# Optimization experiments

Measured on AMD Instinct MI355X. Metric: run time of the kernel, lower is better.

Reference implementation:

```python
import jax, jax.numpy as jnp
import numpy as np

B, N, T, DM, H, M = 32, 207, 24, 64, 8, 32
E = 2 * DM  # true input feature dim (2*dmodel per the reshape in the source)


def setup_inputs() -> dict:
    rng = jax.random.key(0)
    ks = jax.random.split(rng, 10)
    s = 0.05  # scale params to keep activations numerically sane
    query = jax.random.normal(ks[0], (B, N, T, E), jnp.float32)
    key = jax.random.normal(ks[1], (B, N, T, E), jnp.float32)
    value = jax.random.normal(ks[2], (B, N, T, E), jnp.float32)
    # causal temporal mask, broadcast over batch/node/head; True = masked out
    atten_mask = jnp.broadcast_to(jnp.triu(jnp.ones((T, T), bool), 1), (B, N, 1, T, T))
    qp1 = jax.random.normal(ks[3], (N * DM, M), jnp.float32) * s
    qp2 = jax.random.normal(ks[4], (M, 4 * DM), jnp.float32) * s
    kp1 = jax.random.normal(ks[5], (N * DM, M), jnp.float32) * s
    kp2 = jax.random.normal(ks[6], (M, 4 * DM), jnp.float32) * s
    vp1 = jax.random.normal(ks[7], (N * DM, M), jnp.float32) * s
    vp2 = jax.random.normal(ks[8], (M, 4 * DM), jnp.float32) * s
    out_W = jax.random.normal(ks[9], (E, DM), jnp.float32) * s
    out_b = jnp.zeros((DM,), jnp.float32)
    return dict(query=query, key=key, value=value, atten_mask=atten_mask,
                qp1=qp1, qp2=qp2, kp1=kp1, kp2=kp2, vp1=vp1, vp2=vp2,
                out_W=out_W, out_b=out_b, num_heads=H)


def reference(query, key, value, atten_mask, qp1, qp2, kp1, kp2, vp1, vp2, out_W, out_b, num_heads):
    b, n, t, e = query.shape

    def proj(x, p1, p2):
        # low-rank factored per-node projection: (N*dmodel, M) @ (M, 4*dmodel) -> (N, E, E)
        P = (p1 @ p2).reshape(n, e, e)
        y = jnp.einsum('bnti,nik->bntk', x, P)
        return jax.nn.relu(y).reshape(b, n, t, num_heads, -1)

    q = proj(query, qp1, qp2)   # (B,N,T,H,d)
    k = proj(key, kp1, kp2)
    v = proj(value, vp1, vp2)

    scale = 1.0 / np.sqrt(q.shape[-1]).astype(np.float32)
    scores = jnp.einsum('bnthe,bnshe->bnhts', q, k)          # (B,N,H,T,S)
    scores = jnp.where(atten_mask, -jnp.inf, scores)          # masked_fill before scaling
    attn = jax.nn.softmax(scale * scores, axis=-1)            # dropout disabled (eval)
    out = jnp.einsum('bnhts,bnshd->bnthd', attn, v).reshape(b, n, t, -1)
    out = jax.nn.relu(out @ out_W + out_b)                    # (B,N,T,dmodel)
    return out, attn
```

## Files before the change

### kernel.cpp

```cpp
#include <hip/hip_runtime.h>
#include <hip/hip_bf16.h>

#define Bn 32
#define Nn 207
#define Tt 24
#define Ee 128
#define Hh 8
#define Dm 64
#define Mm 32
#define NBN (Bn * Nn)
#define PT ((size_t)Nn * 16384)

typedef __attribute__((ext_vector_type(8))) short bf16x8;
typedef __attribute__((ext_vector_type(4))) float f32x4;

__device__ __forceinline__ unsigned swz256(unsigned a) { return a ^ (((a >> 8) & 7u) << 4); }
__device__ __forceinline__ unsigned swz64(unsigned a)  { return a ^ (((a >> 7) & 3u) << 4); }
__device__ __forceinline__ unsigned f2b(float f) {
  union { float f; unsigned u; } x; x.f = f;
  unsigned u = x.u;
  return ((u + 0x7FFFu + ((u >> 16) & 1u)) >> 16) & 0xFFFFu;
}

__global__ __launch_bounds__(256) void build_P_frag3(
    const float* __restrict__ qp1, const float* __restrict__ qp2,
    const float* __restrict__ kp1, const float* __restrict__ kp2,
    const float* __restrict__ vp1, const float* __restrict__ vp2,
    unsigned short* __restrict__ Pt) {
  const int tau = blockIdx.y;
  const float* p1 = (tau == 0) ? qp1 : (tau == 1) ? kp1 : vp1;
  const float* p2 = (tau == 0) ? qp2 : (tau == 1) ? kp2 : vp2;
  unsigned short* dst = Pt + (size_t)tau * PT;
  const int bid = blockIdx.x;
  const int n = bid >> 3;
  const int r8 = bid & 7;
  const int ks = r8 >> 1;
  const int chunk = ((r8 & 1) << 1) + (threadIdx.x >> 7);
  const int col = threadIdx.x & 127;
  const int base_i = ks * 32 + chunk * 8;
  const float* p1r = p1 + (size_t)(n * 64 + (base_i >> 1)) * Mm;
  const float* p2a = p2 + col;
  const float* p2b = p2 + 128 + col;
  float acc[8] = {};
#pragma unroll
  for (int m = 0; m < Mm; ++m) {
    float a = p2a[m * 256], b = p2b[m * 256];
#pragma unroll
    for (int jj = 0; jj < 4; ++jj) {
      float pv = p1r[jj * Mm + m];
      acc[2 * jj]     = fmaf(pv, a, acc[2 * jj]);
      acc[2 * jj + 1] = fmaf(pv, b, acc[2 * jj + 1]);
    }
  }
  const int nt = col >> 4;
  const int lane = (chunk << 4) | (col & 15);
  union { unsigned short u[8]; uint4 v; } w;
#pragma unroll
  for (int j = 0; j < 8; ++j) w.u[j] = (unsigned short)f2b(acc[j]);
  *(uint4*)(dst + (size_t)(((n * 8 + nt) * 4 + ks) * 64 + lane) * 8) = w.v;
}

__global__ __launch_bounds__(256) void build_W_frag(const float* __restrict__ W,
                                                    unsigned short* __restrict__ Wt) {
  for (int idx = threadIdx.x; idx < 1024; idx += 256) {
    int lane = idx & 63, ks = (idx >> 6) & 3, nt = idx >> 8;
    union { unsigned short u[8]; uint4 v; } w;
#pragma unroll
    for (int j = 0; j < 8; ++j)
      w.u[j] = (unsigned short)f2b(W[(size_t)(ks * 32 + (lane >> 4) * 8 + j) * 64 + nt * 16 + (lane & 15)]);
    *(uint4*)(Wt + (size_t)idx * 8) = w.v;
  }
}

__global__ __launch_bounds__(256, 4) void fused_attn(
    const float* __restrict__ Qin, const float* __restrict__ Kin,
    const float* __restrict__ Vin,
    const unsigned short* __restrict__ Ptq, const unsigned short* __restrict__ Ptk,
    const unsigned short* __restrict__ Ptv, const unsigned short* __restrict__ Wt,
    const float* __restrict__ bias,
    float* __restrict__ out, float* __restrict__ attn) {
  __shared__ __align__(16) char smem[32768];
  const int tid = threadIdx.x;
  const int lane = tid & 63;
  const int wv = tid >> 6;
  const int c = lane & 15;
  const int g = lane >> 4;
  const f32x4 zf = {0.f, 0.f, 0.f, 0.f};
  const bf16x8 zb = {0, 0, 0, 0, 0, 0, 0, 0};

  int bx = blockIdx.x;
  bx = (bx & 7) * 828 + (bx >> 3);
  const int n = bx >> 5;
  const int b = bx & 31;
  const size_t xbase = (size_t)(b * Nn + n) * (Tt * Ee);

  {
    uint4 z4 = {0, 0, 0, 0};
    *(uint4*)(smem + 24576 + tid * 32) = z4;
    *(uint4*)(smem + 24576 + tid * 32 + 16) = z4;
    const float* src[2] = {Qin + xbase, Kin + xbase};
#pragma unroll
    for (int w = 0; w < 2; ++w)
#pragma unroll
      for (int it = 0; it < 3; ++it) {
        int e4 = tid + 256 * it;
        float4 xv = *(const float4*)(src[w] + (size_t)e4 * 4);
        unsigned a = swz256((unsigned)((e4 >> 5) * 256 + (e4 & 31) * 8));
        uint2 pk;
        pk.x = f2b(xv.x) | (f2b(xv.y) << 16);
        pk.y = f2b(xv.z) | (f2b(xv.w) << 16);
        *(uint2*)(smem + w * 6144 + a) = pk;
      }
  }
  __syncthreads();

  {
    const unsigned short* Pts[2] = {Ptq, Ptk};
#pragma unroll
    for (int w = 0; w < 2; ++w) {
      const unsigned short* Pf = Pts[w];
      f32x4 acc[2][2] = {{zf, zf}, {zf, zf}};
#pragma unroll
      for (int ks = 0; ks < 4; ++ks) {
        bf16x8 Bf[2], Af[2];
#pragma unroll
        for (int ntl = 0; ntl < 2; ++ntl)
          Bf[ntl] = *(const bf16x8*)(Pf + (size_t)(((n * 8 + (wv * 2 + ntl)) * 4 + ks) * 64 + lane) * 8);
#pragma unroll
        for (int mt = 0; mt < 2; ++mt) {
          int row = mt * 16 + c; row = row < 24 ? row : 23;
          Af[mt] = *(const bf16x8*)(smem + w * 6144 + swz256((unsigned)(row * 256 + ks * 64 + g * 16)));
        }
        __builtin_amdgcn_s_setprio(1);
#pragma unroll
        for (int mt = 0; mt < 2; ++mt)
#pragma unroll
          for (int ntl = 0; ntl < 2; ++ntl)
            acc[mt][ntl] = __builtin_amdgcn_mfma_f32_16x16x32_bf16(Af[mt], Bf[ntl], acc[mt][ntl], 0, 0, 0);
        __builtin_amdgcn_s_setprio(0);
      }
      const float postscale = (w == 0) ? 0.25f : 1.0f;
      char* dst = smem + 12288 + w * 6144;
#pragma unroll
      for (int mt = 0; mt < 2; ++mt)
#pragma unroll
        for (int r = 0; r < 4; ++r) {
          int row = mt * 16 + g * 4 + r;
          if (row < 24) {
#pragma unroll
            for (int ntl = 0; ntl < 2; ++ntl) {
              int col = (wv * 2 + ntl) * 16 + c;
              *(unsigned short*)(dst + swz256((unsigned)(row * 256 + col * 2))) =
                  (unsigned short)f2b(fmaxf(acc[mt][ntl][r], 0.f) * postscale);
            }
          }
        }
    }
  }

  float4 xvr[3];
#pragma unroll
  for (int it = 0; it < 3; ++it)
    xvr[it] = *(const float4*)(Vin + xbase + (size_t)(tid + 256 * it) * 4);
  __syncthreads();

  f32x4 sc[2][2][2];
#pragma unroll
  for (int hh = 0; hh < 2; ++hh) {
    int h = wv * 2 + hh;
    bf16x8 Aq[2], Bk[2];
#pragma unroll
    for (int mt = 0; mt < 2; ++mt) {
      int row = mt * 16 + c; row = row < 24 ? row : 23;
      Aq[mt] = zb;
      if (lane < 32) Aq[mt] = *(const bf16x8*)(smem + 12288 + swz256((unsigned)(row * 256 + (h * 16 + g * 8) * 2)));
    }
#pragma unroll
    for (int st = 0; st < 2; ++st) {
      int row = st * 16 + c; row = row < 24 ? row : 23;
      Bk[st] = zb;
      if (lane < 32) Bk[st] = *(const bf16x8*)(smem + 18432 + swz256((unsigned)(row * 256 + (h * 16 + g * 8) * 2)));
    }
    __builtin_amdgcn_s_setprio(1);
#pragma unroll
    for (int mt = 0; mt < 2; ++mt)
#pragma unroll
      for (int st = 0; st < 2; ++st)
        sc[hh][mt][st] = __builtin_amdgcn_mfma_f32_16x16x32_bf16(Aq[mt], Bk[st], zf, 0, 0, 0);
    __builtin_amdgcn_s_setprio(0);
  }
  __syncthreads();

  {
    const size_t abase = (size_t)(b * Nn + n) * (Hh * Tt * Tt);
#pragma unroll
    for (int hh = 0; hh < 2; ++hh) {
      int h = wv * 2 + hh;
#pragma unroll
      for (int mt = 0; mt < 2; ++mt)
#pragma unroll
        for (int r = 0; r < 4; ++r) {
          int t = mt * 16 + g * 4 + r;
          float e0 = (c <= t)      ? __expf(sc[hh][mt][0][r]) : 0.f;
          float e1 = (16 + c <= t) ? __expf(sc[hh][mt][1][r]) : 0.f;
          float s2 = e0 + e1;
          s2 += __shfl_xor(s2, 1);
          s2 += __shfl_xor(s2, 2);
          s2 += __shfl_xor(s2, 4);
          s2 += __shfl_xor(s2, 8);
          float inv = 1.0f / s2;
          float p0 = e0 * inv, p1 = e1 * inv;
          if (t < 24) {
            float* ap = attn + abase + (size_t)h * (Tt * Tt) + t * Tt;
            ap[c] = p0;
            if (c < 8) ap[16 + c] = p1;
            char* q = smem + 12288;
            *(unsigned short*)(q + swz64((unsigned)(h * 1536 + t * 64 + c * 2)))        = (unsigned short)f2b(p0);
            *(unsigned short*)(q + swz64((unsigned)(h * 1536 + t * 64 + (16 + c) * 2))) = (unsigned short)f2b(p1);
          }
        }
    }
#pragma unroll
    for (int it = 0; it < 3; ++it) {
      int e4 = tid + 256 * it;
      unsigned a = swz256((unsigned)((e4 >> 5) * 256 + (e4 & 31) * 8));
      uint2 pk;
      pk.x = f2b(xvr[it].x) | (f2b(xvr[it].y) << 16);
      pk.y = f2b(xvr[it].z) | (f2b(xvr[it].w) << 16);
      *(uint2*)(smem + 6144 + a) = pk;
    }
  }
  __syncthreads();

  {
    f32x4 acc[2][2] = {{zf, zf}, {zf, zf}};
#pragma unroll
    for (int ks = 0; ks < 4; ++ks) {
      bf16x8 Bf[2], Af[2];
#pragma unroll
      for (int ntl = 0; ntl < 2; ++ntl)
        Bf[ntl] = *(const bf16x8*)(Ptv + (size_t)(((n * 8 + (wv * 2 + ntl)) * 4 + ks) * 64 + lane) * 8);
#pragma unroll
      for (int mt = 0; mt < 2; ++mt) {
        int row = mt * 16 + c; row = row < 24 ? row : 23;
        Af[mt] = *(const bf16x8*)(smem + 6144 + swz256((unsigned)(row * 256 + ks * 64 + g * 16)));
      }
      __builtin_amdgcn_s_setprio(1);
#pragma unroll
      for (int mt = 0; mt < 2; ++mt)
#pragma unroll
        for (int ntl = 0; ntl < 2; ++ntl)
          acc[mt][ntl] = __builtin_amdgcn_mfma_f32_16x16x32_bf16(Af[mt], Bf[ntl], acc[mt][ntl], 0, 0, 0);
      __builtin_amdgcn_s_setprio(0);
    }
#pragma unroll
    for (int mt = 0; mt < 2; ++mt)
#pragma unroll
      for (int r = 0; r < 4; ++r) {
        int srow = mt * 16 + g * 4 + r;
        if (srow < 24) {
#pragma unroll
          for (int ntl = 0; ntl < 2; ++ntl) {
            int dcol = (wv * 2 + ntl) * 16 + c;
            *(unsigned short*)(smem + 24576 + swz64((unsigned)(dcol * 64 + srow * 2))) =
                (unsigned short)f2b(fmaxf(acc[mt][ntl][r], 0.f));
          }
        }
      }
  }
  __syncthreads();

  {
    f32x4 pv[2][2];
#pragma unroll
    for (int hh = 0; hh < 2; ++hh) {
      int h = wv * 2 + hh;
      bf16x8 Bv = *(const bf16x8*)(smem + 24576 + swz64((unsigned)((h * 16 + c) * 64 + g * 16)));
#pragma unroll
      for (int mt = 0; mt < 2; ++mt) {
        int row = mt * 16 + c; row = row < 24 ? row : 23;
        bf16x8 Ap = *(const bf16x8*)(smem + 12288 + swz64((unsigned)(h * 1536 + row * 64 + g * 16)));
        pv[hh][mt] = __builtin_amdgcn_mfma_f32_16x16x32_bf16(Ap, Bv, zf, 0, 0, 0);
      }
    }
#pragma unroll
    for (int hh = 0; hh < 2; ++hh) {
      int h = wv * 2 + hh;
#pragma unroll
      for (int mt = 0; mt < 2; ++mt)
#pragma unroll
        for (int r = 0; r < 4; ++r) {
          int t = mt * 16 + g * 4 + r;
          if (t < 24)
            *(unsigned short*)(smem + swz256((unsigned)(t * 256 + (h * 16 + c) * 2))) =
                (unsigned short)f2b(pv[hh][mt][r]);
        }
    }
  }
  __syncthreads();

  {
    f32x4 acc2[2] = {zf, zf};
#pragma unroll
    for (int ks = 0; ks < 4; ++ks) {
      bf16x8 Bw = *(const bf16x8*)(Wt + (size_t)((wv * 4 + ks) * 64 + lane) * 8);
      bf16x8 Af[2];
#pragma unroll
      for (int mt = 0; mt < 2; ++mt) {
        int row = mt * 16 + c; row = row < 24 ? row : 23;
        Af[mt] = *(const bf16x8*)(smem + swz256((unsigned)(row * 256 + ks * 64 + g * 16)));
      }
      __builtin_amdgcn_s_setprio(1);
#pragma unroll
      for (int mt = 0; mt < 2; ++mt)
        acc2[mt] = __builtin_amdgcn_mfma_f32_16x16x32_bf16(Af[mt], Bw, acc2[mt], 0, 0, 0);
      __builtin_amdgcn_s_setprio(0);
    }
    int j = wv * 16 + c;
    float bj = bias[j];
    const size_t obase = (size_t)(b * Nn + n) * (Tt * Dm);
#pragma unroll
    for (int mt = 0; mt < 2; ++mt)
#pragma unroll
      for (int r = 0; r < 4; ++r) {
        int t = mt * 16 + g * 4 + r;
        if (t < 24) out[obase + (size_t)t * Dm + j] = fmaxf(acc2[mt][r] + bj, 0.f);
      }
  }
}

extern "C" void kernel_launch(void* const* d_in, const int* in_sizes, int n_in,
                              void* d_out, int out_size, void* d_ws, size_t ws_size,
                              hipStream_t stream) {
  const float* query = (const float*)d_in[0];
  const float* key   = (const float*)d_in[1];
  const float* value = (const float*)d_in[2];
  const float* qp1 = (const float*)d_in[4];
  const float* qp2 = (const float*)d_in[5];
  const float* kp1 = (const float*)d_in[6];
  const float* kp2 = (const float*)d_in[7];
  const float* vp1 = (const float*)d_in[8];
  const float* vp2 = (const float*)d_in[9];
  const float* out_W = (const float*)d_in[10];
  const float* out_b = (const float*)d_in[11];

  unsigned short* Pt  = (unsigned short*)d_ws;
  unsigned short* Wtf = Pt + 3 * PT;

  float* out = (float*)d_out;
  float* attn = out + (size_t)NBN * Tt * Dm;

  build_P_frag3<<<dim3(Nn * 8, 3), 256, 0, stream>>>(qp1, qp2, kp1, kp2, vp1, vp2, Pt);
  build_W_frag<<<1, 256, 0, stream>>>(out_W, Wtf);
  fused_attn<<<NBN, 256, 0, stream>>>(query, key, value,
                                      Pt, Pt + PT, Pt + 2 * PT, Wtf,
                                      out_b, out, attn);
}
```

Measured before the change: 159.2 us.

## Fuse V projection into QK projection stage and use hardware bf16 pack converts

```diff
diff --git a/kernel.cpp b/kernel.cpp
--- a/kernel.cpp
+++ b/kernel.cpp
@@ -16,10 +16,13 @@
 
 __device__ __forceinline__ unsigned swz256(unsigned a) { return a ^ (((a >> 8) & 7u) << 4); }
 __device__ __forceinline__ unsigned swz64(unsigned a)  { return a ^ (((a >> 7) & 3u) << 4); }
-__device__ __forceinline__ unsigned f2b(float f) {
-  union { float f; unsigned u; } x; x.f = f;
-  unsigned u = x.u;
-  return ((u + 0x7FFFu + ((u >> 16) & 1u)) >> 16) & 0xFFFFu;
+__device__ __forceinline__ unsigned cvtpk(float lo, float hi) {
+  unsigned r;
+  asm("v_cvt_pk_bf16_f32 %0, %1, %2" : "=v"(r) : "v"(lo), "v"(hi));
+  return r;
+}
+__device__ __forceinline__ unsigned short f2bs(float f) {
+  return (unsigned short)cvtpk(f, f);
 }
 
 __global__ __launch_bounds__(256) void build_P_frag3(
@@ -54,9 +57,9 @@
   }
   const int nt = col >> 4;
   const int lane = (chunk << 4) | (col & 15);
-  union { unsigned short u[8]; uint4 v; } w;
-#pragma unroll
-  for (int j = 0; j < 8; ++j) w.u[j] = (unsigned short)f2b(acc[j]);
+  union { unsigned u[4]; uint4 v; } w;
+#pragma unroll
+  for (int jj = 0; jj < 4; ++jj) w.u[jj] = cvtpk(acc[2 * jj], acc[2 * jj + 1]);
   *(uint4*)(dst + (size_t)(((n * 8 + nt) * 4 + ks) * 64 + lane) * 8) = w.v;
 }
 
@@ -64,10 +67,13 @@
                                                     unsigned short* __restrict__ Wt) {
   for (int idx = threadIdx.x; idx < 1024; idx += 256) {
     int lane = idx & 63, ks = (idx >> 6) & 3, nt = idx >> 8;
-    union { unsigned short u[8]; uint4 v; } w;
-#pragma unroll
-    for (int j = 0; j < 8; ++j)
-      w.u[j] = (unsigned short)f2b(W[(size_t)(ks * 32 + (lane >> 4) * 8 + j) * 64 + nt * 16 + (lane & 15)]);
+    union { unsigned u[4]; uint4 v; } w;
+#pragma unroll
+    for (int jj = 0; jj < 4; ++jj) {
+      float a = W[(size_t)(ks * 32 + (lane >> 4) * 8 + 2 * jj) * 64 + nt * 16 + (lane & 15)];
+      float b = W[(size_t)(ks * 32 + (lane >> 4) * 8 + 2 * jj + 1) * 64 + nt * 16 + (lane & 15)];
+      w.u[jj] = cvtpk(a, b);
+    }
     *(uint4*)(Wt + (size_t)idx * 8) = w.v;
   }
 }
@@ -79,7 +85,7 @@
     const unsigned short* __restrict__ Ptv, const unsigned short* __restrict__ Wt,
     const float* __restrict__ bias,
     float* __restrict__ out, float* __restrict__ attn) {
-  __shared__ __align__(16) char smem[32768];
+  __shared__ __align__(16) char smem[38912];
   const int tid = threadIdx.x;
   const int lane = tid & 63;
   const int wv = tid >> 6;
@@ -96,29 +102,28 @@
 
   {
     uint4 z4 = {0, 0, 0, 0};
-    *(uint4*)(smem + 24576 + tid * 32) = z4;
-    *(uint4*)(smem + 24576 + tid * 32 + 16) = z4;
-    const float* src[2] = {Qin + xbase, Kin + xbase};
-#pragma unroll
-    for (int w = 0; w < 2; ++w)
+    *(uint4*)(smem + 30720 + tid * 32) = z4;
+    *(uint4*)(smem + 30720 + tid * 32 + 16) = z4;
+    const float* src[3] = {Qin + xbase, Kin + xbase, Vin + xbase};
+#pragma unroll
+    for (int w = 0; w < 3; ++w)
 #pragma unroll
       for (int it = 0; it < 3; ++it) {
         int e4 = tid + 256 * it;
         float4 xv = *(const float4*)(src[w] + (size_t)e4 * 4);
         unsigned a = swz256((unsigned)((e4 >> 5) * 256 + (e4 & 31) * 8));
         uint2 pk;
-        pk.x = f2b(xv.x) | (f2b(xv.y) << 16);
-        pk.y = f2b(xv.z) | (f2b(xv.w) << 16);
+        pk.x = cvtpk(xv.x, xv.y);
+        pk.y = cvtpk(xv.z, xv.w);
         *(uint2*)(smem + w * 6144 + a) = pk;
       }
   }
   __syncthreads();
 
   {
-    const unsigned short* Pts[2] = {Ptq, Ptk};
-#pragma unroll
-    for (int w = 0; w < 2; ++w) {
-      const unsigned short* Pf = Pts[w];
+#pragma unroll
+    for (int w = 0; w < 3; ++w) {
+      const unsigned short* Pf = (w == 0) ? Ptq : (w == 1) ? Ptk : Ptv;
       f32x4 acc[2][2] = {{zf, zf}, {zf, zf}};
 #pragma unroll
       for (int ks = 0; ks < 4; ++ks) {
@@ -139,55 +144,40 @@
             acc[mt][ntl] = __builtin_amdgcn_mfma_f32_16x16x32_bf16(Af[mt], Bf[ntl], acc[mt][ntl], 0, 0, 0);
         __builtin_amdgcn_s_setprio(0);
       }
-      const float postscale = (w == 0) ? 0.25f : 1.0f;
-      char* dst = smem + 12288 + w * 6144;
-#pragma unroll
-      for (int mt = 0; mt < 2; ++mt)
-#pragma unroll
-        for (int r = 0; r < 4; ++r) {
-          int row = mt * 16 + g * 4 + r;
-          if (row < 24) {
-#pragma unroll
-            for (int ntl = 0; ntl < 2; ++ntl) {
-              int col = (wv * 2 + ntl) * 16 + c;
-              *(unsigned short*)(dst + swz256((unsigned)(row * 256 + col * 2))) =
-                  (unsigned short)f2b(fmaxf(acc[mt][ntl][r], 0.f) * postscale);
+      if (w < 2) {
+        const float postscale = (w == 0) ? 0.25f : 1.0f;
+        char* dst = smem + 18432 + w * 6144;
+#pragma unroll
+        for (int mt = 0; mt < 2; ++mt)
+#pragma unroll
+          for (int r = 0; r < 4; ++r) {
+            int row = mt * 16 + g * 4 + r;
+            if (row < 24) {
+#pragma unroll
+              for (int ntl = 0; ntl < 2; ++ntl) {
+                int col = (wv * 2 + ntl) * 16 + c;
+                *(unsigned short*)(dst + swz256((unsigned)(row * 256 + col * 2))) =
+                    f2bs(fmaxf(acc[mt][ntl][r], 0.f) * postscale);
+              }
             }
           }
-        }
-    }
-  }
-
-  float4 xvr[3];
-#pragma unroll
-  for (int it = 0; it < 3; ++it)
-    xvr[it] = *(const float4*)(Vin + xbase + (size_t)(tid + 256 * it) * 4);
-  __syncthreads();
-
-  f32x4 sc[2][2][2];
-#pragma unroll
-  for (int hh = 0; hh < 2; ++hh) {
-    int h = wv * 2 + hh;
-    bf16x8 Aq[2], Bk[2];
-#pragma unroll
-    for (int mt = 0; mt < 2; ++mt) {
-      int row = mt * 16 + c; row = row < 24 ? row : 23;
-      Aq[mt] = zb;
-      if (lane < 32) Aq[mt] = *(const bf16x8*)(smem + 12288 + swz256((unsigned)(row * 256 + (h * 16 + g * 8) * 2)));
-    }
-#pragma unroll
-    for (int st = 0; st < 2; ++st) {
-      int row = st * 16 + c; row = row < 24 ? row : 23;
-      Bk[st] = zb;
-      if (lane < 32) Bk[st] = *(const bf16x8*)(smem + 18432 + swz256((unsigned)(row * 256 + (h * 16 + g * 8) * 2)));
-    }
-    __builtin_amdgcn_s_setprio(1);
-#pragma unroll
-    for (int mt = 0; mt < 2; ++mt)
-#pragma unroll
-      for (int st = 0; st < 2; ++st)
-        sc[hh][mt][st] = __builtin_amdgcn_mfma_f32_16x16x32_bf16(Aq[mt], Bk[st], zf, 0, 0, 0);
-    __builtin_amdgcn_s_setprio(0);
+      } else {
+#pragma unroll
+        for (int mt = 0; mt < 2; ++mt)
+#pragma unroll
+          for (int r = 0; r < 4; ++r) {
+            int srow = mt * 16 + g * 4 + r;
+            if (srow < 24) {
+#pragma unroll
+              for (int ntl = 0; ntl < 2; ++ntl) {
+                int dcol = (wv * 2 + ntl) * 16 + c;
+                *(unsigned short*)(smem + 30720 + swz64((unsigned)(dcol * 64 + srow * 2))) =
+                    f2bs(fmaxf(acc[mt][ntl][r], 0.f));
+              }
+            }
+          }
+      }
+    }
   }
   __syncthreads();
 
@@ -196,13 +186,34 @@
 #pragma unroll
     for (int hh = 0; hh < 2; ++hh) {
       int h = wv * 2 + hh;
+      bf16x8 Aq[2], Bk[2];
+#pragma unroll
+      for (int mt = 0; mt < 2; ++mt) {
+        int row = mt * 16 + c; row = row < 24 ? row : 23;
+        Aq[mt] = zb;
+        if (lane < 32) Aq[mt] = *(const bf16x8*)(smem + 18432 + swz256((unsigned)(row * 256 + (h * 16 + g * 8) * 2)));
+      }
+#pragma unroll
+      for (int st = 0; st < 2; ++st) {
+        int row = st * 16 + c; row = row < 24 ? row : 23;
+        Bk[st] = zb;
+        if (lane < 32) Bk[st] = *(const bf16x8*)(smem + 24576 + swz256((unsigned)(row * 256 + (h * 16 + g * 8) * 2)));
+      }
+      f32x4 sc[2][2];
+      __builtin_amdgcn_s_setprio(1);
+#pragma unroll
+      for (int mt = 0; mt < 2; ++mt)
+#pragma unroll
+        for (int st = 0; st < 2; ++st)
+          sc[mt][st] = __builtin_amdgcn_mfma_f32_16x16x32_bf16(Aq[mt], Bk[st], zf, 0, 0, 0);
+      __builtin_amdgcn_s_setprio(0);
 #pragma unroll
       for (int mt = 0; mt < 2; ++mt)
 #pragma unroll
         for (int r = 0; r < 4; ++r) {
           int t = mt * 16 + g * 4 + r;
-          float e0 = (c <= t)      ? __expf(sc[hh][mt][0][r]) : 0.f;
-          float e1 = (16 + c <= t) ? __expf(sc[hh][mt][1][r]) : 0.f;
+          float e0 = (c <= t)      ? __expf(sc[mt][0][r]) : 0.f;
+          float e1 = (16 + c <= t) ? __expf(sc[mt][1][r]) : 0.f;
           float s2 = e0 + e1;
           s2 += __shfl_xor(s2, 1);
           s2 += __shfl_xor(s2, 2);
@@ -214,72 +225,24 @@
             float* ap = attn + abase + (size_t)h * (Tt * Tt) + t * Tt;
             ap[c] = p0;
             if (c < 8) ap[16 + c] = p1;
-            char* q = smem + 12288;
-            *(unsigned short*)(q + swz64((unsigned)(h * 1536 + t * 64 + c * 2)))        = (unsigned short)f2b(p0);
-            *(unsigned short*)(q + swz64((unsigned)(h * 1536 + t * 64 + (16 + c) * 2))) = (unsigned short)f2b(p1);
+            *(unsigned short*)(smem + swz64((unsigned)(h * 1536 + t * 64 + c * 2)))        = f2bs(p0);
+            *(unsigned short*)(smem + swz64((unsigned)(h * 1536 + t * 64 + (16 + c) * 2))) = f2bs(p1);
           }
         }
     }
-#pragma unroll
-    for (int it = 0; it < 3; ++it) {
-      int e4 = tid + 256 * it;
-      unsigned a = swz256((unsigned)((e4 >> 5) * 256 + (e4 & 31) * 8));
-      uint2 pk;
-      pk.x = f2b(xvr[it].x) | (f2b(xvr[it].y) << 16);
-      pk.y = f2b(xvr[it].z) | (f2b(xvr[it].w) << 16);
-      *(uint2*)(smem + 6144 + a) = pk;
-    }
   }
   __syncthreads();
 
   {
-    f32x4 acc[2][2] = {{zf, zf}, {zf, zf}};
-#pragma unroll
-    for (int ks = 0; ks < 4; ++ks) {
-      bf16x8 Bf[2], Af[2];
-#pragma unroll
-      for (int ntl = 0; ntl < 2; ++ntl)
-        Bf[ntl] = *(const bf16x8*)(Ptv + (size_t)(((n * 8 + (wv * 2 + ntl)) * 4 + ks) * 64 + lane) * 8);
+    f32x4 pv[2][2];
+#pragma unroll
+    for (int hh = 0; hh < 2; ++hh) {
+      int h = wv * 2 + hh;
+      bf16x8 Bv = *(const bf16x8*)(smem + 30720 + swz64((unsigned)((h * 16 + c) * 64 + g * 16)));
 #pragma unroll
       for (int mt = 0; mt < 2; ++mt) {
         int row = mt * 16 + c; row = row < 24 ? row : 23;
-        Af[mt] = *(const bf16x8*)(smem + 6144 + swz256((unsigned)(row * 256 + ks * 64 + g * 16)));
-      }
-      __builtin_amdgcn_s_setprio(1);
-#pragma unroll
-      for (int mt = 0; mt < 2; ++mt)
-#pragma unroll
-        for (int ntl = 0; ntl < 2; ++ntl)
-          acc[mt][ntl] = __builtin_amdgcn_mfma_f32_16x16x32_bf16(Af[mt], Bf[ntl], acc[mt][ntl], 0, 0, 0);
-      __builtin_amdgcn_s_setprio(0);
-    }
-#pragma unroll
-    for (int mt = 0; mt < 2; ++mt)
-#pragma unroll
-      for (int r = 0; r < 4; ++r) {
-        int srow = mt * 16 + g * 4 + r;
-        if (srow < 24) {
-#pragma unroll
-          for (int ntl = 0; ntl < 2; ++ntl) {
-            int dcol = (wv * 2 + ntl) * 16 + c;
-            *(unsigned short*)(smem + 24576 + swz64((unsigned)(dcol * 64 + srow * 2))) =
-                (unsigned short)f2b(fmaxf(acc[mt][ntl][r], 0.f));
-          }
-        }
-      }
-  }
-  __syncthreads();
-
-  {
-    f32x4 pv[2][2];
-#pragma unroll
-    for (int hh = 0; hh < 2; ++hh) {
-      int h = wv * 2 + hh;
-      bf16x8 Bv = *(const bf16x8*)(smem + 24576 + swz64((unsigned)((h * 16 + c) * 64 + g * 16)));
-#pragma unroll
-      for (int mt = 0; mt < 2; ++mt) {
-        int row = mt * 16 + c; row = row < 24 ? row : 23;
-        bf16x8 Ap = *(const bf16x8*)(smem + 12288 + swz64((unsigned)(h * 1536 + row * 64 + g * 16)));
+        bf16x8 Ap = *(const bf16x8*)(smem + swz64((unsigned)(h * 1536 + row * 64 + g * 16)));
         pv[hh][mt] = __builtin_amdgcn_mfma_f32_16x16x32_bf16(Ap, Bv, zf, 0, 0, 0);
       }
     }
@@ -292,8 +255,8 @@
         for (int r = 0; r < 4; ++r) {
           int t = mt * 16 + g * 4 + r;
           if (t < 24)
-            *(unsigned short*)(smem + swz256((unsigned)(t * 256 + (h * 16 + c) * 2))) =
-                (unsigned short)f2b(pv[hh][mt][r]);
+            *(unsigned short*)(smem + 12288 + swz256((unsigned)(t * 256 + (h * 16 + c) * 2))) =
+                f2bs(pv[hh][mt][r]);
         }
     }
   }
@@ -308,7 +271,7 @@
 #pragma unroll
       for (int mt = 0; mt < 2; ++mt) {
         int row = mt * 16 + c; row = row < 24 ? row : 23;
-        Af[mt] = *(const bf16x8*)(smem + swz256((unsigned)(row * 256 + ks * 64 + g * 16)));
+        Af[mt] = *(const bf16x8*)(smem + 12288 + swz256((unsigned)(row * 256 + ks * 64 + g * 16)));
       }
       __builtin_amdgcn_s_setprio(1);
 #pragma unroll
```

After: 169.1 us. 6.2% more time.
